# Optimization experiments

Hardware: AMD Instinct MI355X
Metric: run time of the kernel (lower is better)

The kernel has to match this reference:

```python
import jax, jax.numpy as jnp
import numpy as np

T, B, D, ATTN_D, K = 128, 2048, 1024, 1024, 8


def setup_inputs() -> dict:
    key = jax.random.key(0)
    k1, k2, k3, k4 = jax.random.split(key, 4)
    h_context = jax.random.normal(k1, (T, B, D), dtype=jnp.float32)
    offsets = jax.random.randint(k2, (B,), 0, T, dtype=jnp.int32)
    stc_lens = jnp.full((B,), T, dtype=jnp.int32)
    # one separator per sample at position T: segment [0, T], identical math to no-sep case
    sep_lst = jnp.full((B, 1), T, dtype=jnp.int32)
    # xavier-normal-ish init for the attention MLP weights (torch Linear layout: [out, in])
    W1 = jax.random.normal(k3, (ATTN_D, D), dtype=jnp.float32) * np.sqrt(2.0 / (D + ATTN_D))
    W2 = jax.random.normal(k4, (1, ATTN_D), dtype=jnp.float32) * np.sqrt(2.0 / (ATTN_D + 1))
    return {"h_context": h_context, "offsets": offsets, "stc_lens": stc_lens,
            "sep_lst": sep_lst, "no_local": 0, "W1": W1, "W2": W2}


def reference(h_context, offsets, stc_lens, sep_lst, no_local, W1, W2):
    # h_context: [T, B, D] (seq-first). no_local is unused (as in the original forward).
    Kw = 8
    Tn, Bn, Dn = h_context.shape
    L = 2 * Kw  # max window length: range(pos-K, pos+K) has at most 2K elements

    # Segment bounds: with a single separator per sample, pos is either in
    # segment [0, sep] or in segment [sep+1, stc_len] (mirrors the loop in forward).
    sep = sep_lst[:, 0]
    in_seg1 = offsets <= sep
    start = jnp.where(in_seg1, jnp.maximum(offsets - Kw, 0), jnp.maximum(offsets - Kw, sep + 1))
    end = jnp.where(in_seg1, jnp.minimum(offsets + Kw, sep), jnp.minimum(offsets + Kw, stc_lens))

    idx = start[:, None] + jnp.arange(L, dtype=start.dtype)  # [B, L]
    valid = idx < end[:, None]                               # [B, L] True = real token
    idx_c = jnp.clip(idx, 0, Tn - 1)

    # Irregular per-sample gather: blk[b, l] = h_context[idx[b, l], b]
    blk = h_context[idx_c, jnp.arange(Bn)[:, None]]          # [B, L, D]
    blk = jnp.where(valid[..., None], blk, jnp.zeros((), blk.dtype))  # zero padding (= F.pad)

    blk_t = blk.transpose(1, 0, 2)                           # [L, B, D] (matches h_context_blk)
    # attn_trans: Linear(D->attn_d) -> tanh -> Linear(attn_d->1) -> Softmax(dim=1)
    a = jnp.tanh(jnp.einsum('lbd,ad->lba', blk_t, W1))       # [L, B, attn_d]
    s = jnp.einsum('lba,oa->lbo', a, W2)                     # [L, B, 1]
    s = jax.nn.softmax(s, axis=1)                            # softmax over batch dim (dim=1)
    score = jnp.mean(s, axis=2)                              # [L, B]

    # masked softmax over the window dim (dim=0); padded rows -> -inf
    score = jnp.where(valid.T, score, -jnp.inf)
    score = jax.nn.softmax(score, axis=0)                    # [L, B]

    # bmm: [B,1,L] @ [B,L,D] -> [B,1,D]
    h_blank = jnp.einsum('lb,bld->bd', score, blk)[:, None, :]
    return h_blank
```

## Files before the change

### kernel.cpp

```cpp
#include <hip/hip_runtime.h>

#define T_DIM 128
#define B_DIM 2048
#define D_DIM 1024
#define KW 8
#define NCOL (B_DIM * 16)

#define PL   2064
#define BUFB (8 * PL)

typedef _Float16 f16x8 __attribute__((ext_vector_type(8)));
typedef _Float16 f16x4 __attribute__((ext_vector_type(4)));
typedef float    f32x16 __attribute__((ext_vector_type(16)));

static __device__ __forceinline__ int imax(int a, int b) { return a > b ? a : b; }
static __device__ __forceinline__ int imin(int a, int b) { return a < b ? a : b; }

__global__ void k_cvt_w1(const float* __restrict__ W1, _Float16* __restrict__ W1f) {
    int i  = blockIdx.x * 256 + threadIdx.x;
    int m  = i >> 6;
    int kc = i & 63;
    const float* src = W1 + (size_t)m * D_DIM + kc * 16;
    float4 x0 = *(const float4*)(src);
    float4 x1 = *(const float4*)(src + 4);
    float4 x2 = *(const float4*)(src + 8);
    float4 x3 = *(const float4*)(src + 12);
    f16x8 h0, h1;
    h0[0] = (_Float16)x0.x; h0[1] = (_Float16)x0.y;
    h0[2] = (_Float16)x0.z; h0[3] = (_Float16)x0.w;
    h0[4] = (_Float16)x1.x; h0[5] = (_Float16)x1.y;
    h0[6] = (_Float16)x1.z; h0[7] = (_Float16)x1.w;
    h1[0] = (_Float16)x2.x; h1[1] = (_Float16)x2.y;
    h1[2] = (_Float16)x2.z; h1[3] = (_Float16)x2.w;
    h1[4] = (_Float16)x3.x; h1[5] = (_Float16)x3.y;
    h1[6] = (_Float16)x3.z; h1[7] = (_Float16)x3.w;
    _Float16* dst = W1f + ((size_t)kc * 1024 + m) * 16;
    *(f16x8*)(dst)     = h0;
    *(f16x8*)(dst + 8) = h1;
}

__launch_bounds__(512, 2)
__global__ void k_gemm(const float* __restrict__ hctx,
                       const int*   __restrict__ offsets,
                       const int*   __restrict__ stc,
                       const int*   __restrict__ sep_l,
                       const _Float16* __restrict__ W1f,
                       const float* __restrict__ W2,
                       float* __restrict__ s_raw) {
    __shared__ __align__(16) char ldsx[2 * BUFB];
    __shared__ float red[8][64];

    int cg   = blockIdx.x;
    int tid  = threadIdx.x;
    int wid  = tid >> 6;
    int lane = tid & 63;
    int lr   = lane & 31;
    int hi   = lane >> 5;

    const float* sbase[4];
    int svalid[4];
    int wr_off[4];
#pragma unroll
    for (int rr = 0; rr < 4; ++rr) {
        int colL = wid * 8 + rr * 2 + hi;
        int col  = cg * 64 + colL;
        int b    = col >> 4;
        int li   = col & 15;
        int off = offsets[b];
        int sep = sep_l[b];
        int st  = stc[b];
        bool in1 = (off <= sep);
        int start = in1 ? imax(off - KW, 0)   : imax(off - KW, sep + 1);
        int end   = in1 ? imin(off + KW, sep) : imin(off + KW, st);
        int idx = start + li;
        svalid[rr] = (idx < end) ? 1 : 0;
        int tc = imin(imax(idx, 0), T_DIM - 1);
        sbase[rr] = hctx + ((size_t)tc * B_DIM + b) * D_DIM + lr * 4;
        wr_off[rr] = (lr >> 2) * PL + ((lr >> 1) & 1) * 1024 + colL * 16 + (lr & 1) * 8;
    }

    const _Float16* ap = W1f + (size_t)(wid * 128 + lr) * 16 + hi * 8;
    int rd_off = hi * 1024 + lr * 16;

    f32x16 acc[4][2];
#pragma unroll
    for (int f = 0; f < 4; ++f)
#pragma unroll
        for (int nf = 0; nf < 2; ++nf)
#pragma unroll
            for (int i = 0; i < 16; ++i) acc[f][nf][i] = 0.f;

    {
        float4 z = {0.f, 0.f, 0.f, 0.f};
#pragma unroll
        for (int rr = 0; rr < 4; ++rr) {
            float4 x = svalid[rr] ? *(const float4*)(sbase[rr]) : z;
            f16x4 h;
            h[0] = (_Float16)x.x; h[1] = (_Float16)x.y;
            h[2] = (_Float16)x.z; h[3] = (_Float16)x.w;
            *(f16x4*)(ldsx + wr_off[rr]) = h;
        }
    }
    __syncthreads();

    f16x8 a_c[4];
#pragma unroll
    for (int f = 0; f < 4; ++f)
        a_c[f] = *(const f16x8*)(ap + f * 512);

    for (int c = 0; c < 8; ++c) {
        int bufr = (c & 1) * BUFB;

        float4 xn[4];
        if (c < 7) {
            int k0 = (c + 1) * 128;
            float4 z = {0.f, 0.f, 0.f, 0.f};
#pragma unroll
            for (int rr = 0; rr < 4; ++rr)
                xn[rr] = svalid[rr] ? *(const float4*)(sbase[rr] + k0) : z;
        }

#pragma unroll
        for (int kcL = 0; kcL < 8; ++kcL) {
            int kc = c * 8 + kcL;
            int kn = (kc + 1) & 63;
            f16x8 a_n[4];
#pragma unroll
            for (int f = 0; f < 4; ++f)
                a_n[f] = *(const f16x8*)(ap + (size_t)kn * 16384 + f * 512);

            const char* bp = ldsx + bufr + kcL * PL + rd_off;
            f16x8 b0 = *(const f16x8*)(bp);
            f16x8 b1 = *(const f16x8*)(bp + 512);

#pragma unroll
            for (int f = 0; f < 4; ++f)
                acc[f][0] = __builtin_amdgcn_mfma_f32_32x32x16_f16(
                    a_c[f], b0, acc[f][0], 0, 0, 0);
#pragma unroll
            for (int f = 0; f < 4; ++f)
                acc[f][1] = __builtin_amdgcn_mfma_f32_32x32x16_f16(
                    a_c[f], b1, acc[f][1], 0, 0, 0);
#pragma unroll
            for (int f = 0; f < 4; ++f) a_c[f] = a_n[f];
        }

        if (c < 7) {
            int bufw = ((c + 1) & 1) * BUFB;
#pragma unroll
            for (int rr = 0; rr < 4; ++rr) {
                f16x4 h;
                h[0] = (_Float16)xn[rr].x; h[1] = (_Float16)xn[rr].y;
                h[2] = (_Float16)xn[rr].z; h[3] = (_Float16)xn[rr].w;
                *(f16x4*)(ldsx + bufw + wr_off[rr]) = h;
            }
        }
        __syncthreads();
    }

    int m_wg = wid * 128;
    float sp0 = 0.f, sp1 = 0.f;
#pragma unroll
    for (int f = 0; f < 4; ++f) {
#pragma unroll
        for (int rg = 0; rg < 4; ++rg) {
            int mbase = m_wg + f * 32 + rg * 8 + hi * 4;
            float4 w2v = *(const float4*)(W2 + mbase);
            float w2a[4] = {w2v.x, w2v.y, w2v.z, w2v.w};
#pragma unroll
            for (int j = 0; j < 4; ++j) {
                float w2 = w2a[j];
                {
                    float x = acc[f][0][rg * 4 + j];
                    float e = __expf(2.f * x);
                    sp0 += w2 * (1.f - 2.f / (e + 1.f));
                }
                {
                    float x = acc[f][1][rg * 4 + j];
                    float e = __expf(2.f * x);
                    sp1 += w2 * (1.f - 2.f / (e + 1.f));
                }
            }
        }
    }
    sp0 += __shfl_xor(sp0, 32, 64);
    sp1 += __shfl_xor(sp1, 32, 64);

    if (hi == 0) {
        red[wid][lr]      = sp0;
        red[wid][32 + lr] = sp1;
    }
    __syncthreads();
    if (tid < 64) {
        float s = 0.f;
#pragma unroll
        for (int w = 0; w < 8; ++w) s += red[w][tid];
        s_raw[cg * 64 + tid] = s;
    }
}

__global__ void k_smax1(const float* __restrict__ s_raw,
                        float* __restrict__ lstats ) {
    int l = blockIdx.x;
    int t = threadIdx.x;
    int lane = t & 63, wid = t >> 6;

    float v[8];
    float mx = -__builtin_inff();
#pragma unroll
    for (int i = 0; i < 8; ++i) {
        int b = i * 256 + t;
        float x = s_raw[b * 16 + l];
        v[i] = x;
        mx = fmaxf(mx, x);
    }
#pragma unroll
    for (int d = 1; d < 64; d <<= 1) mx = fmaxf(mx, __shfl_xor(mx, d, 64));
    __shared__ float rm[4];
    if (lane == 0) rm[wid] = mx;
    __syncthreads();
    mx = fmaxf(fmaxf(rm[0], rm[1]), fmaxf(rm[2], rm[3]));

    float se = 0.f;
#pragma unroll
    for (int i = 0; i < 8; ++i) se += __expf(v[i] - mx);
#pragma unroll
    for (int d = 1; d < 64; d <<= 1) se += __shfl_xor(se, d, 64);
    __shared__ float rs[4];
    if (lane == 0) rs[wid] = se;
    __syncthreads();
    if (t == 0) {
        lstats[l]      = mx;
        lstats[16 + l] = rs[0] + rs[1] + rs[2] + rs[3];
    }
}

__global__ void k_out(const float* __restrict__ hctx,
                      const int*   __restrict__ offsets,
                      const int*   __restrict__ stc,
                      const int*   __restrict__ sep_l,
                      const float* __restrict__ s_raw,
                      const float* __restrict__ lstats,
                      float* __restrict__ out) {
    int b = blockIdx.x;
    int t = threadIdx.x;

    int off = offsets[b];
    int sep = sep_l[b];
    int st  = stc[b];
    bool in1 = (off <= sep);
    int start = in1 ? imax(off - KW, 0)   : imax(off - KW, sep + 1);
    int end   = in1 ? imin(off + KW, sep) : imin(off + KW, st);

    float p[16];
    float m2 = -__builtin_inff();
#pragma unroll
    for (int l = 0; l < 16; ++l) {
        bool valid = (start + l) < end;
        float s = s_raw[b * 16 + l];
        float pl = __expf(s - lstats[l]) / lstats[16 + l];
        p[l] = valid ? pl : -__builtin_inff();
        m2 = fmaxf(m2, p[l]);
    }
    float q[16];
    float qs = 0.f;
#pragma unroll
    for (int l = 0; l < 16; ++l) {
        float e = __expf(p[l] - m2);
        q[l] = e;
        qs += e;
    }
    float rqs = 1.f / qs;

    float4 acc = {0.f, 0.f, 0.f, 0.f};
#pragma unroll
    for (int l = 0; l < 16; ++l) {
        float wl = q[l] * rqs;
        if (wl > 0.f) {
            int tr = imin(imax(start + l, 0), T_DIM - 1);
            float4 x = *((const float4*)(hctx + ((size_t)tr * B_DIM + b) * D_DIM) + t);
            acc.x += wl * x.x; acc.y += wl * x.y;
            acc.z += wl * x.z; acc.w += wl * x.w;
        }
    }
    *((float4*)(out + (size_t)b * D_DIM) + t) = acc;
}

extern "C" void kernel_launch(void* const* d_in, const int* in_sizes, int n_in,
                              void* d_out, int out_size, void* d_ws, size_t ws_size,
                              hipStream_t stream) {
    const float* hctx    = (const float*)d_in[0];
    const int*   offsets = (const int*)d_in[1];
    const int*   stc     = (const int*)d_in[2];
    const int*   sep     = (const int*)d_in[3];
    const float* W1      = (const float*)d_in[5];
    const float* W2      = (const float*)d_in[6];
    float* out = (float*)d_out;

    char* ws = (char*)d_ws;
    _Float16* W1f    = (_Float16*)ws;
    float*    s_raw  = (float*)(ws + (2u << 20));
    float*    lstats = (float*)(ws + (2u << 20) + (128u << 10));

    hipLaunchKernelGGL(k_cvt_w1, dim3(256),  dim3(256), 0, stream, W1, W1f);
    hipLaunchKernelGGL(k_gemm,   dim3(512),  dim3(512), 0, stream,
                       hctx, offsets, stc, sep, W1f, W2, s_raw);
    hipLaunchKernelGGL(k_smax1,  dim3(16),   dim3(256), 0, stream, s_raw, lstats);
    hipLaunchKernelGGL(k_out,    dim3(2048), dim3(256), 0, stream,
                       hctx, offsets, stc, sep, s_raw, lstats, out);
}
```

Baseline: 137.4 us.

## Retile gating GEMM into 128-column blocks split across two M halves

```diff
diff --git a/kernel.cpp b/kernel.cpp
--- a/kernel.cpp
+++ b/kernel.cpp
@@ -6,11 +6,9 @@
 #define KW 8
 #define NCOL (B_DIM * 16)
 
-#define PL   2064
-#define BUFB (8 * PL)
+#define XBUF 32768
 
 typedef _Float16 f16x8 __attribute__((ext_vector_type(8)));
-typedef _Float16 f16x4 __attribute__((ext_vector_type(4)));
 typedef float    f32x16 __attribute__((ext_vector_type(16)));
 
 static __device__ __forceinline__ int imax(int a, int b) { return a > b ? a : b; }
@@ -46,41 +44,41 @@
                        const int*   __restrict__ sep_l,
                        const _Float16* __restrict__ W1f,
                        const float* __restrict__ W2,
-                       float* __restrict__ s_raw) {
-    __shared__ __align__(16) char ldsx[2 * BUFB];
+                       float* __restrict__ s_part ) {
+    __shared__ __align__(16) char ldsx[2 * XBUF];
     __shared__ float red[8][64];
 
-    int cg   = blockIdx.x;
-    int tid  = threadIdx.x;
-    int wid  = tid >> 6;
+    int bid = blockIdx.x;
+    int mt  = bid & 1;
+    int cg  = bid >> 1;
+    int tid = threadIdx.x;
+    int wid = tid >> 6;
     int lane = tid & 63;
-    int lr   = lane & 31;
-    int hi   = lane >> 5;
-
-    const float* sbase[4];
-    int svalid[4];
-    int wr_off[4];
-#pragma unroll
-    for (int rr = 0; rr < 4; ++rr) {
-        int colL = wid * 8 + rr * 2 + hi;
-        int col  = cg * 64 + colL;
-        int b    = col >> 4;
-        int li   = col & 15;
-        int off = offsets[b];
-        int sep = sep_l[b];
-        int st  = stc[b];
-        bool in1 = (off <= sep);
-        int start = in1 ? imax(off - KW, 0)   : imax(off - KW, sep + 1);
-        int end   = in1 ? imin(off + KW, sep) : imin(off + KW, st);
-        int idx = start + li;
-        svalid[rr] = (idx < end) ? 1 : 0;
-        int tc = imin(imax(idx, 0), T_DIM - 1);
-        sbase[rr] = hctx + ((size_t)tc * B_DIM + b) * D_DIM + lr * 4;
-        wr_off[rr] = (lr >> 2) * PL + ((lr >> 1) & 1) * 1024 + colL * 16 + (lr & 1) * 8;
-    }
-
-    const _Float16* ap = W1f + (size_t)(wid * 128 + lr) * 16 + hi * 8;
-    int rd_off = hi * 1024 + lr * 16;
+    int lr = lane & 31;
+    int hi = lane >> 5;
+    int mg = wid >> 1;
+    int ng = wid & 1;
+
+    int s_col = tid & 127;
+    int ks    = tid >> 7;
+    int col = cg * 128 + s_col;
+    int b   = col >> 4;
+    int li  = col & 15;
+    int off = offsets[b];
+    int sep = sep_l[b];
+    int st  = stc[b];
+    bool in1 = (off <= sep);
+    int start = in1 ? imax(off - KW, 0)   : imax(off - KW, sep + 1);
+    int end   = in1 ? imin(off + KW, sep) : imin(off + KW, st);
+    int idx = start + li;
+    bool valid = (idx < end);
+    int tc = imin(imax(idx, 0), T_DIM - 1);
+    const float* sbase = hctx + ((size_t)tc * B_DIM + b) * D_DIM + ks * 32;
+    int s_woff = ks * 8192 + s_col * 16;
+
+    const _Float16* ap = W1f + (size_t)(mt * 512 + mg * 128 + lr) * 16 + hi * 8;
+
+    int x_roff = hi * 2048 + (ng * 64 + lr) * 16;
 
     f32x16 acc[4][2];
 #pragma unroll
@@ -91,93 +89,94 @@
             for (int i = 0; i < 16; ++i) acc[f][nf][i] = 0.f;
 
     {
+        float4 xv[8];
         float4 z = {0.f, 0.f, 0.f, 0.f};
 #pragma unroll
-        for (int rr = 0; rr < 4; ++rr) {
-            float4 x = svalid[rr] ? *(const float4*)(sbase[rr]) : z;
-            f16x4 h;
-            h[0] = (_Float16)x.x; h[1] = (_Float16)x.y;
-            h[2] = (_Float16)x.z; h[3] = (_Float16)x.w;
-            *(f16x4*)(ldsx + wr_off[rr]) = h;
-        }
+        for (int q = 0; q < 8; ++q)
+            xv[q] = valid ? *(const float4*)(sbase + q * 4) : z;
+#pragma unroll
+        for (int p = 0; p < 2; ++p)
+#pragma unroll
+            for (int jh = 0; jh < 2; ++jh) {
+                float4 u = xv[p * 4 + jh * 2], v = xv[p * 4 + jh * 2 + 1];
+                f16x8 h;
+                h[0] = (_Float16)u.x; h[1] = (_Float16)u.y;
+                h[2] = (_Float16)u.z; h[3] = (_Float16)u.w;
+                h[4] = (_Float16)v.x; h[5] = (_Float16)v.y;
+                h[6] = (_Float16)v.z; h[7] = (_Float16)v.w;
+                *(f16x8*)(ldsx + s_woff + p * 4096 + jh * 2048) = h;
+            }
     }
     __syncthreads();
 
-    f16x8 a_c[4];
-#pragma unroll
-    for (int f = 0; f < 4; ++f)
-        a_c[f] = *(const f16x8*)(ap + f * 512);
-
     for (int c = 0; c < 8; ++c) {
-        int bufr = (c & 1) * BUFB;
-
-        float4 xn[4];
+        int cur = (c & 1) * XBUF;
+
+        float4 xn[8];
         if (c < 7) {
-            int k0 = (c + 1) * 128;
             float4 z = {0.f, 0.f, 0.f, 0.f};
-#pragma unroll
-            for (int rr = 0; rr < 4; ++rr)
-                xn[rr] = svalid[rr] ? *(const float4*)(sbase[rr] + k0) : z;
+            const float* sp = sbase + (c + 1) * 128;
+#pragma unroll
+            for (int q = 0; q < 8; ++q)
+                xn[q] = valid ? *(const float4*)(sp + q * 4) : z;
         }
 
 #pragma unroll
         for (int kcL = 0; kcL < 8; ++kcL) {
             int kc = c * 8 + kcL;
-            int kn = (kc + 1) & 63;
-            f16x8 a_n[4];
+            f16x8 a[4];
 #pragma unroll
             for (int f = 0; f < 4; ++f)
-                a_n[f] = *(const f16x8*)(ap + (size_t)kn * 16384 + f * 512);
-
-            const char* bp = ldsx + bufr + kcL * PL + rd_off;
-            f16x8 b0 = *(const f16x8*)(bp);
-            f16x8 b1 = *(const f16x8*)(bp + 512);
-
+                a[f] = *(const f16x8*)(ap + (size_t)kc * 16384 + f * 512);
+            f16x8 x0 = *(const f16x8*)(ldsx + cur + kcL * 4096 + x_roff);
+            f16x8 x1 = *(const f16x8*)(ldsx + cur + kcL * 4096 + x_roff + 512);
 #pragma unroll
             for (int f = 0; f < 4; ++f)
                 acc[f][0] = __builtin_amdgcn_mfma_f32_32x32x16_f16(
-                    a_c[f], b0, acc[f][0], 0, 0, 0);
+                    a[f], x0, acc[f][0], 0, 0, 0);
 #pragma unroll
             for (int f = 0; f < 4; ++f)
                 acc[f][1] = __builtin_amdgcn_mfma_f32_32x32x16_f16(
-                    a_c[f], b1, acc[f][1], 0, 0, 0);
-#pragma unroll
-            for (int f = 0; f < 4; ++f) a_c[f] = a_n[f];
+                    a[f], x1, acc[f][1], 0, 0, 0);
         }
 
         if (c < 7) {
-            int bufw = ((c + 1) & 1) * BUFB;
-#pragma unroll
-            for (int rr = 0; rr < 4; ++rr) {
-                f16x4 h;
-                h[0] = (_Float16)xn[rr].x; h[1] = (_Float16)xn[rr].y;
-                h[2] = (_Float16)xn[rr].z; h[3] = (_Float16)xn[rr].w;
-                *(f16x4*)(ldsx + bufw + wr_off[rr]) = h;
-            }
+            int nxt = ((c + 1) & 1) * XBUF;
+#pragma unroll
+            for (int p = 0; p < 2; ++p)
+#pragma unroll
+                for (int jh = 0; jh < 2; ++jh) {
+                    float4 u = xn[p * 4 + jh * 2], v = xn[p * 4 + jh * 2 + 1];
+                    f16x8 h;
+                    h[0] = (_Float16)u.x; h[1] = (_Float16)u.y;
+                    h[2] = (_Float16)u.z; h[3] = (_Float16)u.w;
+                    h[4] = (_Float16)v.x; h[5] = (_Float16)v.y;
+                    h[6] = (_Float16)v.z; h[7] = (_Float16)v.w;
+                    *(f16x8*)(ldsx + nxt + s_woff + p * 4096 + jh * 2048) = h;
+                }
         }
         __syncthreads();
     }
 
-    int m_wg = wid * 128;
     float sp0 = 0.f, sp1 = 0.f;
 #pragma unroll
     for (int f = 0; f < 4; ++f) {
 #pragma unroll
         for (int rg = 0; rg < 4; ++rg) {
-            int mbase = m_wg + f * 32 + rg * 8 + hi * 4;
+            int mbase = mt * 512 + mg * 128 + f * 32 + rg * 8 + hi * 4;
             float4 w2v = *(const float4*)(W2 + mbase);
             float w2a[4] = {w2v.x, w2v.y, w2v.z, w2v.w};
 #pragma unroll
             for (int j = 0; j < 4; ++j) {
                 float w2 = w2a[j];
                 {
-                    float x = acc[f][0][rg * 4 + j];
-                    float e = __expf(2.f * x);
+                    float xv = acc[f][0][rg * 4 + j];
+                    float e = __expf(2.f * xv);
                     sp0 += w2 * (1.f - 2.f / (e + 1.f));
                 }
                 {
-                    float x = acc[f][1][rg * 4 + j];
-                    float e = __expf(2.f * x);
+                    float xv = acc[f][1][rg * 4 + j];
+                    float e = __expf(2.f * xv);
                     sp1 += w2 * (1.f - 2.f / (e + 1.f));
                 }
             }
@@ -191,15 +190,18 @@
         red[wid][32 + lr] = sp1;
     }
     __syncthreads();
-    if (tid < 64) {
+    if (tid < 128) {
+        int ngc = tid >> 6;
+        int cl  = tid & 63;
         float s = 0.f;
 #pragma unroll
-        for (int w = 0; w < 8; ++w) s += red[w][tid];
-        s_raw[cg * 64 + tid] = s;
-    }
-}
-
-__global__ void k_smax1(const float* __restrict__ s_raw,
+        for (int mgi = 0; mgi < 4; ++mgi) s += red[mgi * 2 + ngc][cl];
+        s_part[(size_t)mt * NCOL + cg * 128 + tid] = s;
+    }
+}
+
+__global__ void k_smax1(const float* __restrict__ s_part,
+                        float* __restrict__ s_raw,
                         float* __restrict__ lstats ) {
     int l = blockIdx.x;
     int t = threadIdx.x;
@@ -210,8 +212,9 @@
 #pragma unroll
     for (int i = 0; i < 8; ++i) {
         int b = i * 256 + t;
-        float x = s_raw[b * 16 + l];
+        float x = s_part[b * 16 + l] + s_part[NCOL + b * 16 + l];
         v[i] = x;
+        s_raw[b * 16 + l] = x;
         mx = fmaxf(mx, x);
     }
 #pragma unroll
@@ -299,13 +302,15 @@
 
     char* ws = (char*)d_ws;
     _Float16* W1f    = (_Float16*)ws;
-    float*    s_raw  = (float*)(ws + (2u << 20));
-    float*    lstats = (float*)(ws + (2u << 20) + (128u << 10));
+    float*    s_part = (float*)(ws + (2u << 20));
+    float*    s_raw  = (float*)(ws + (2u << 20) + (256u << 10));
+    float*    lstats = (float*)(ws + (2u << 20) + (384u << 10));
 
     hipLaunchKernelGGL(k_cvt_w1, dim3(256),  dim3(256), 0, stream, W1, W1f);
     hipLaunchKernelGGL(k_gemm,   dim3(512),  dim3(512), 0, stream,
-                       hctx, offsets, stc, sep, W1f, W2, s_raw);
-    hipLaunchKernelGGL(k_smax1,  dim3(16),   dim3(256), 0, stream, s_raw, lstats);
+                       hctx, offsets, stc, sep, W1f, W2, s_part);
+    hipLaunchKernelGGL(k_smax1,  dim3(16),   dim3(256), 0, stream,
+                       s_part, s_raw, lstats);
     hipLaunchKernelGGL(k_out,    dim3(2048), dim3(256), 0, stream,
                        hctx, offsets, stc, sep, s_raw, lstats, out);
 }
```

New measurement: 187.7 us. +36.5%, slower.
